# Optimization experiments

Hardware: AMD Instinct MI355X
Metric: run time of the kernel (lower is better)

## Reference

```python
import jax, jax.numpy as jnp
import numpy as np

N_NODES = 1_000_000
N_EDGES = 8_000_000
C_IN, C_HID, C_OUT = 64, 64, 32


def setup_inputs() -> dict:
    key = jax.random.key(0)
    ks = jax.random.split(key, 8)
    x = jax.random.normal(ks[0], (N_NODES, C_IN), dtype=jnp.float32)
    edge_index = jax.random.randint(ks[1], (2, N_EDGES), 0, N_NODES, dtype=jnp.int64)
    edge_weight = jax.random.uniform(ks[2], (N_EDGES,), dtype=jnp.float32)
    # ChebConv(K=1) params: one Linear(in, out, bias=False) + separate bias (glorot/zeros in torch; random here)
    s0 = 1.0 / np.sqrt(C_IN)
    s1 = 1.0 / np.sqrt(C_HID)
    W0 = jax.random.uniform(ks[3], (C_HID, C_IN), dtype=jnp.float32, minval=-s0, maxval=s0)
    W1 = jax.random.uniform(ks[4], (C_HID, C_HID), dtype=jnp.float32, minval=-s1, maxval=s1)
    W2 = jax.random.uniform(ks[5], (C_OUT, C_HID), dtype=jnp.float32, minval=-s1, maxval=s1)
    b0 = jax.random.uniform(ks[6], (C_HID,), dtype=jnp.float32, minval=-s0, maxval=s0)
    b1 = jax.random.uniform(ks[7], (C_HID,), dtype=jnp.float32, minval=-s1, maxval=s1)
    b2 = jnp.zeros((C_OUT,), dtype=jnp.float32)
    return {"x": x, "edge_index": edge_index, "edge_weight": edge_weight,
            "W0": W0, "b0": b0, "W1": W1, "b1": b1, "W2": W2, "b2": b2}


def reference(x, edge_index, edge_weight, W0, b0, W1, b1, W2, b2):
    # PyG ChebConv with K=1: out = Linear(x) + bias; the propagate (gather/scatter)
    # branch is only taken for K >= 2, so edge_index/edge_weight do not affect the output.
    del edge_index, edge_weight
    h = jax.nn.relu(x @ W0.T + b0)   # layer 0 + relu  [N, C_HID]
    h = jax.nn.relu(h @ W1.T + b1)   # layer 1 + relu  [N, C_HID]
    return h @ W2.T + b2             # final layer, no relu  [N, C_OUT]
```

## Files before the change

kernel.cpp:

```cpp
#include <hip/hip_runtime.h>

typedef __bf16 bf16x4 __attribute__((ext_vector_type(4)));
typedef __bf16 bf16x8 __attribute__((ext_vector_type(8)));
typedef float f32x4 __attribute__((ext_vector_type(4)));

__device__ __forceinline__ f32x4 mfma16(bf16x8 a, bf16x8 b, f32x4 c) {
    return __builtin_amdgcn_mfma_f32_16x16x32_bf16(a, b, c, 0, 0, 0);
}

__global__ __launch_bounds__(256) void cheb_mlp_kernel(
    const float* __restrict__ x,
    const float* __restrict__ W0, const float* __restrict__ b0v,
    const float* __restrict__ W1, const float* __restrict__ b1v,
    const float* __restrict__ W2, const float* __restrict__ b2v,
    float* __restrict__ out, int n_nodes)
{
    __shared__ __bf16 w0s[64][72];
    __shared__ __bf16 w1s[64][72];
    __shared__ __bf16 w2s[32][72];
    __shared__ float bias0[64], bias1[64], bias2[32];
    __shared__ __bf16 hbuf[4][16][72];

    const int tid = threadIdx.x;

    for (int i = tid; i < 64 * 64; i += 256) {
        int r = i >> 6, c = i & 63;
        w0s[r][c] = (__bf16)W0[i];
        w1s[r][c] = (__bf16)W1[i];
    }
    for (int i = tid; i < 32 * 64; i += 256) {
        w2s[i >> 6][i & 63] = (__bf16)W2[i];
    }
    if (tid < 64)      { bias0[tid] = b0v[tid]; bias1[tid] = b1v[tid]; }
    else if (tid < 96) { bias2[tid - 64] = b2v[tid - 64]; }
    __syncthreads();

    const int wave = tid >> 6;
    const int lane = tid & 63;
    const int lr = lane & 15;
    const int lg = lane >> 4;

    bf16x8 fw0[4][2], fw2[2][2];
#pragma unroll
    for (int t = 0; t < 4; ++t)
#pragma unroll
        for (int s = 0; s < 2; ++s)
            fw0[t][s] = *(const bf16x8*)&w0s[t * 16 + lr][s * 32 + lg * 8];
#pragma unroll
    for (int t = 0; t < 2; ++t)
#pragma unroll
        for (int s = 0; s < 2; ++s)
            fw2[t][s] = *(const bf16x8*)&w2s[t * 16 + lr][s * 32 + lg * 8];

    const int wave_base = blockIdx.x * 128 + wave * 32;
    if (wave_base >= n_nodes) return;
    const int rem = (n_nodes - wave_base) >> 4;
    const int nt = rem < 2 ? rem : 2;

    const float* xbase = x + (size_t)(wave_base + lr) * 64 + lg * 8;

    f32x4 cx0, cx1, cx2, cx3;
    {
        const float* xp = xbase;
        cx0 = *(const f32x4*)(xp);
        cx1 = *(const f32x4*)(xp + 4);
        cx2 = *(const f32x4*)(xp + 32);
        cx3 = *(const f32x4*)(xp + 36);
    }

#pragma unroll
    for (int mt = 0; mt < 2; ++mt) {
        if (mt >= nt) break;
        const int m_cur = wave_base + mt * 16;

        f32x4 nx0, nx1, nx2, nx3;
        const bool has_next = (mt + 1 < nt);
        if (has_next) {
            const float* xp = xbase + (size_t)(mt + 1) * 1024;
            nx0 = *(const f32x4*)(xp);
            nx1 = *(const f32x4*)(xp + 4);
            nx2 = *(const f32x4*)(xp + 32);
            nx3 = *(const f32x4*)(xp + 36);
        }

        bf16x8 ax0, ax1;
#pragma unroll
        for (int j = 0; j < 4; ++j) {
            ax0[j]     = (__bf16)cx0[j];
            ax0[j + 4] = (__bf16)cx1[j];
            ax1[j]     = (__bf16)cx2[j];
            ax1[j + 4] = (__bf16)cx3[j];
        }

        f32x4 acc[4];
#pragma unroll
        for (int t = 0; t < 4; ++t) {
            acc[t] = *(const f32x4*)&bias0[t * 16 + lg * 4];
            acc[t] = mfma16(fw0[t][0], ax0, acc[t]);
            acc[t] = mfma16(fw0[t][1], ax1, acc[t]);
        }
#pragma unroll
        for (int t = 0; t < 4; ++t) {
            bf16x4 pk;
#pragma unroll
            for (int r = 0; r < 4; ++r) {
                float v = acc[t][r];
                pk[r] = (__bf16)(v > 0.f ? v : 0.f);
            }
            *(bf16x4*)&hbuf[wave][lr][t * 16 + lg * 4] = pk;
        }

        bf16x8 ah0 = *(const bf16x8*)&hbuf[wave][lr][lg * 8];
        bf16x8 ah1 = *(const bf16x8*)&hbuf[wave][lr][32 + lg * 8];
#pragma unroll
        for (int t = 0; t < 4; ++t) {
            bf16x8 f0 = *(const bf16x8*)&w1s[t * 16 + lr][lg * 8];
            bf16x8 f1 = *(const bf16x8*)&w1s[t * 16 + lr][32 + lg * 8];
            acc[t] = *(const f32x4*)&bias1[t * 16 + lg * 4];
            acc[t] = mfma16(f0, ah0, acc[t]);
            acc[t] = mfma16(f1, ah1, acc[t]);
        }
#pragma unroll
        for (int t = 0; t < 4; ++t) {
            bf16x4 pk;
#pragma unroll
            for (int r = 0; r < 4; ++r) {
                float v = acc[t][r];
                pk[r] = (__bf16)(v > 0.f ? v : 0.f);
            }
            *(bf16x4*)&hbuf[wave][lr][t * 16 + lg * 4] = pk;
        }

        bf16x8 ag0 = *(const bf16x8*)&hbuf[wave][lr][lg * 8];
        bf16x8 ag1 = *(const bf16x8*)&hbuf[wave][lr][32 + lg * 8];
#pragma unroll
        for (int t = 0; t < 2; ++t) {
            f32x4 a2 = *(const f32x4*)&bias2[t * 16 + lg * 4];
            a2 = mfma16(fw2[t][0], ag0, a2);
            a2 = mfma16(fw2[t][1], ag1, a2);
            __builtin_nontemporal_store(a2, (f32x4*)&out[(size_t)(m_cur + lr) * 32 + t * 16 + lg * 4]);
        }

        if (has_next) { cx0 = nx0; cx1 = nx1; cx2 = nx2; cx3 = nx3; }
    }
}

extern "C" void kernel_launch(void* const* d_in, const int* in_sizes, int n_in,
                              void* d_out, int out_size, void* d_ws, size_t ws_size,
                              hipStream_t stream) {
    const float* x  = (const float*)d_in[0];
    const float* W0 = (const float*)d_in[3];
    const float* b0 = (const float*)d_in[4];
    const float* W1 = (const float*)d_in[5];
    const float* b1 = (const float*)d_in[6];
    const float* W2 = (const float*)d_in[7];
    const float* b2 = (const float*)d_in[8];
    float* out = (float*)d_out;

    const int n_nodes = in_sizes[0] / 64;
    const int grid = (n_nodes + 127) / 128;
    cheb_mlp_kernel<<<grid, 256, 0, stream>>>(x, W0, b0, W1, b1, W2, b2, out, n_nodes);
}
```

Measured before the change: 76.67 us.

## Switch to persistent grid-stride loop over 16-row tiles with fixed grid

Replaces the one-block-per-128-rows launch with a fixed grid of 1024 blocks whose waves loop over 16-row tiles in grid-stride order, prefetching the next tile's x while computing the current one. This amortizes the per-block setup of converting and staging W0/W1/W2 into LDS and loading fragments, which was repeated for every ~7800 blocks. The risk is less memory-level parallelism per CU and tail imbalance, and rows beyond a multiple of 16 are not handled (fine for 1M nodes).

```diff
diff --git a/kernel.cpp b/kernel.cpp
--- a/kernel.cpp
+++ b/kernel.cpp
@@ -52,35 +52,32 @@
         for (int s = 0; s < 2; ++s)
             fw2[t][s] = *(const bf16x8*)&w2s[t * 16 + lr][s * 32 + lg * 8];
 
-    const int wave_base = blockIdx.x * 128 + wave * 32;
-    if (wave_base >= n_nodes) return;
-    const int rem = (n_nodes - wave_base) >> 4;
-    const int nt = rem < 2 ? rem : 2;
+    const int total_tiles = n_nodes >> 4;
+    const int g = blockIdx.x * 4 + wave;
+    const int wstride = gridDim.x * 4;
+    if (g >= total_tiles) return;
+    const int niter = (total_tiles - g + wstride - 1) / wstride;
 
-    const float* xbase = x + (size_t)(wave_base + lr) * 64 + lg * 8;
+    const size_t tile_step = (size_t)wstride * 16 * 64;
+    const float* xp = x + (size_t)g * 16 * 64 + (size_t)lr * 64 + lg * 8;
 
-    f32x4 cx0, cx1, cx2, cx3;
-    {
-        const float* xp = xbase;
-        cx0 = *(const f32x4*)(xp);
-        cx1 = *(const f32x4*)(xp + 4);
-        cx2 = *(const f32x4*)(xp + 32);
-        cx3 = *(const f32x4*)(xp + 36);
-    }
+    f32x4 cx0 = *(const f32x4*)(xp);
+    f32x4 cx1 = *(const f32x4*)(xp + 4);
+    f32x4 cx2 = *(const f32x4*)(xp + 32);
+    f32x4 cx3 = *(const f32x4*)(xp + 36);
 
-#pragma unroll
-    for (int mt = 0; mt < 2; ++mt) {
-        if (mt >= nt) break;
-        const int m_cur = wave_base + mt * 16;
+    int m_cur = g * 16;
+    const int m_step = wstride * 16;
 
+    for (int it = 0; it < niter; ++it) {
         f32x4 nx0, nx1, nx2, nx3;
-        const bool has_next = (mt + 1 < nt);
+        const bool has_next = (it + 1 < niter);
         if (has_next) {
-            const float* xp = xbase + (size_t)(mt + 1) * 1024;
-            nx0 = *(const f32x4*)(xp);
-            nx1 = *(const f32x4*)(xp + 4);
-            nx2 = *(const f32x4*)(xp + 32);
-            nx3 = *(const f32x4*)(xp + 36);
+            const float* np = xp + tile_step;
+            nx0 = *(const f32x4*)(np);
+            nx1 = *(const f32x4*)(np + 4);
+            nx2 = *(const f32x4*)(np + 32);
+            nx3 = *(const f32x4*)(np + 36);
         }
 
         bf16x8 ax0, ax1;
@@ -142,6 +139,8 @@
         }
 
         if (has_next) { cx0 = nx0; cx1 = nx1; cx2 = nx2; cx3 = nx3; }
+        xp += tile_step;
+        m_cur += m_step;
     }
 }
 
@@ -158,6 +157,6 @@
     float* out = (float*)d_out;
 
     const int n_nodes = in_sizes[0] / 64;
-    const int grid = (n_nodes + 127) / 128;
+    const int grid = 1024;
     cheb_mlp_kernel<<<grid, 256, 0, stream>>>(x, W0, b0, W1, b1, W2, b2, out, n_nodes);
 }
```

Result: faster. 64.13 us (-16.4%).
